# Kernel tuning notes

Measured on AMD Instinct MI355X. Metric: run time of the kernel, lower is better.

The kernel has to match this reference:

```python
import jax, jax.numpy as jnp
import numpy as np

B, S, H = 2, 2048, 1024
NQ, NKV, HD, RANK = 16, 4, 64, 8
THETA = 10000.0
LORA_SCALE = 16 / RANK  # alpha / rank = 2.0
ATTN_SCALE = 1.0 / np.sqrt(HD)


def setup_inputs() -> dict:
    key = jax.random.key(0)
    ks = jax.random.split(key, 14)
    n = lambda k, shape, s: jax.random.normal(k, shape, jnp.float32) * s
    return {
        "x": n(ks[0], (B, S, H), 1.0),
        # nn.Linear weights: [out_features, in_features], y = x @ W.T (scaled small for stability)
        "Wq": n(ks[1], (NQ * HD, H), 0.02),
        "Wk": n(ks[2], (NKV * HD, H), 0.02),
        "Wv": n(ks[3], (NKV * HD, H), 0.02),
        "Wo": n(ks[4], (H, NQ * HD), 0.02),
        "qA": n(ks[5], (RANK, H), 0.05), "qB": n(ks[6], (NQ * HD, RANK), 0.05),
        "kA": n(ks[7], (RANK, H), 0.05), "kB": n(ks[8], (NKV * HD, RANK), 0.05),
        "vA": n(ks[9], (RANK, H), 0.05), "vB": n(ks[10], (NKV * HD, RANK), 0.05),
        "oA": n(ks[11], (RANK, NQ * HD), 0.05), "oB": n(ks[12], (H, RANK), 0.05),
    }


def _lora_proj(x, W, A, Bm):
    # x @ W.T + ((x @ A.T) @ B.T) * lora_scaling
    return x @ W.T + ((x @ A.T) @ Bm.T) * LORA_SCALE


def _rope(x, cos_h, sin_h):
    # x: [b, h, s, d]; even/odd interleaved split, concatenated output (matches torch ref)
    x1, x2 = x[..., ::2], x[..., 1::2]
    return jnp.concatenate([x1 * cos_h - x2 * sin_h, x1 * sin_h + x2 * cos_h], axis=-1)


def _forward(x, Wq, Wk, Wv, Wo, qA, qB, kA, kB, vA, vB, oA, oB):
    b, s, _ = x.shape
    q = _lora_proj(x, Wq, qA, qB).reshape(b, s, NQ, HD).transpose(0, 2, 1, 3)
    k = _lora_proj(x, Wk, kA, kB).reshape(b, s, NKV, HD).transpose(0, 2, 1, 3)
    v = _lora_proj(x, Wv, vA, vB).reshape(b, s, NKV, HD).transpose(0, 2, 1, 3)

    inv_freq = 1.0 / (THETA ** (jnp.arange(0, HD, 2, dtype=jnp.float32) / HD))  # [HD/2]
    freqs = jnp.arange(s, dtype=jnp.float32)[:, None] * inv_freq[None, :]  # [s, HD/2]
    cos_h = jnp.cos(freqs)[None, None]  # [1,1,s,HD/2]
    sin_h = jnp.sin(freqs)[None, None]
    q = _rope(q, cos_h, sin_h)
    k = _rope(k, cos_h, sin_h)

    rep = NQ // NKV  # GQA: repeat_interleave along head axis
    k = jnp.repeat(k, rep, axis=1)
    v = jnp.repeat(v, rep, axis=1)

    attn = jax.nn.softmax(jnp.einsum('bhqd,bhkd->bhqk', q, k) * ATTN_SCALE, axis=-1)
    out = jnp.einsum('bhqk,bhkd->bhqd', attn, v)
    out = out.transpose(0, 2, 1, 3).reshape(b, s, NQ * HD)
    return _lora_proj(out, Wo, oA, oB)


def reference(x, Wq, Wk, Wv, Wo, qA, qB, kA, kB, vA, vB, oA, oB):
    return _forward(x, Wq, Wk, Wv, Wo, qA, qB, kA, kB, vA, vB, oA, oB)
```

## Files before the change

### kernel.cpp

```cpp
#include <hip/hip_runtime.h>

typedef _Float16 f16;
typedef __attribute__((ext_vector_type(8))) _Float16 f16x8;
typedef __attribute__((ext_vector_type(4))) float f32x4;

#define DI __device__ __forceinline__
#define MFMA16(a, b, c) __builtin_amdgcn_mfma_f32_16x16x32_f16(a, b, c, 0, 0, 0)

constexpr int BB = 2, SS = 2048, HH = 1024;
constexpr int NQ = 16, NKV = 4, HD = 64;
constexpr int NTOK = BB * SS;
constexpr int NQKV = NQ*HD + 2*NKV*HD;

DI f32x4 zero4() { f32x4 z = {0.f, 0.f, 0.f, 0.f}; return z; }

DI float fexp2(float x) {
#if __has_builtin(__builtin_amdgcn_exp2f)
  return __builtin_amdgcn_exp2f(x);
#else
  return exp2f(x);
#endif
}

DI unsigned pk2(float a, float b) {
#if __has_builtin(__builtin_amdgcn_cvt_pkrtz)
  typedef __fp16 fp16v2 __attribute__((ext_vector_type(2)));
  union { fp16v2 h; unsigned u; } c;
  c.h = __builtin_amdgcn_cvt_pkrtz(a, b);
  return c.u;
#else
  union { f16 h[2]; unsigned u; } c;
  c.h[0] = (f16)a; c.h[1] = (f16)b; return c.u;
#endif
}

DI void glds16(const void* g, void* l) {
  __builtin_amdgcn_global_load_lds((const __attribute__((address_space(1))) void*)g,
                                   (__attribute__((address_space(3))) void*)l, 16, 0, 0);
}

DI int shuf32(int i) {
  return (i & ~31) | (((i >> 2) & 3) << 3) | (i & 3) | (((i >> 4) & 1) << 2);
}

__global__ __launch_bounds__(256) void prep_kernel(
    const float* __restrict__ x,
    const float* __restrict__ Wq, const float* __restrict__ Wk,
    const float* __restrict__ Wv, const float* __restrict__ Wo,
    const float* __restrict__ qA, const float* __restrict__ qB,
    const float* __restrict__ kA, const float* __restrict__ kB,
    const float* __restrict__ vA, const float* __restrict__ vB,
    const float* __restrict__ oA, const float* __restrict__ oB,
    f16* __restrict__ xh, f16* __restrict__ Wqkv, f16* __restrict__ Woe,
    float* __restrict__ ctab, float* __restrict__ stab) {
  int idx = blockIdx.x * 256 + threadIdx.x;
  if (idx < NQKV * HH) {
    int n = idx >> 10, hcol = idx & 1023;
    const float *Am, *Bm; float wv; int nn;
    if (n < 1024)      { nn = n;        wv = Wq[idx];              Am = qA; Bm = qB; }
    else if (n < 1280) { nn = n - 1024; wv = Wk[nn*1024 + hcol];   Am = kA; Bm = kB; }
    else               { nn = n - 1280; wv = Wv[nn*1024 + hcol];   Am = vA; Bm = vB; }
    float s = 0.f;
#pragma unroll
    for (int r = 0; r < 8; ++r) s += Bm[nn*8 + r] * Am[r*1024 + hcol];
    Wqkv[shuf32(idx)] = (f16)(wv + 2.0f * s);
  } else if ((idx -= NQKV * HH) < 1024 * 1024) {
    int n = idx >> 10, hcol = idx & 1023;
    float s = 0.f;
#pragma unroll
    for (int r = 0; r < 8; ++r) s += oB[n*8 + r] * oA[r*1024 + hcol];
    Woe[shuf32(idx)] = (f16)(Wo[idx] + 2.0f * s);
  } else if ((idx -= 1024 * 1024) < NTOK * HH) {
    xh[shuf32(idx)] = (f16)x[idx];
  } else if ((idx -= NTOK * HH) < SS * 32) {
    int s = idx >> 5, d = idx & 31;
    float inv = expf(-(float)d * 0.28782313662425583f);
    float ang = (float)s * inv;
    ctab[idx] = cosf(ang);
    stab[idx] = sinf(ang);
  }
}

template<typename OUT_T>
__global__ __launch_bounds__(256, 2) void gemm_bt(const f16* __restrict__ A, const f16* __restrict__ Bw,
                                                  OUT_T* __restrict__ C, int M, int N, int K) {
  __shared__ char lds[65536];
  const int nt = N >> 7;
  const int nwg = (M >> 7) * nt;
  int bid = blockIdx.x;
  const int cpx = nwg >> 3;
  bid = (bid & 7) * cpx + (bid >> 3);
  const int m0 = (bid / nt) << 7;
  const int n0 = (bid % nt) << 7;
  const int tid = threadIdx.x;
  const int lane = tid & 63;
  const int w = tid >> 6, wr = w >> 1, wc = w & 1;
  const int l15 = lane & 15, g = (lane >> 4) & 3;
  const char* Ab = (const char*)A;
  const char* Bb = (const char*)Bw;
  const size_t Kb = (size_t)K * 2;
  const int srow = tid >> 3;
  const int scol = (tid & 7) << 4;

  auto stage = [&](int kt, int bs) {
    char* ab = lds + bs * 32768;
    char* bbuf = ab + 16384;
    const size_t kbyte = (size_t)kt << 7;
#pragma unroll
    for (int s = 0; s < 4; ++s) {
      int row = (s << 5) + srow;
      glds16(Ab + (size_t)(m0 + row) * Kb + kbyte + (scol ^ ((row & 7) << 4)),
             ab + (s << 12) + (w << 10));
    }
#pragma unroll
    for (int s = 0; s < 4; ++s) {
      int row = (s << 5) + srow;
      glds16(Bb + (size_t)(n0 + row) * Kb + kbyte + (scol ^ ((row & 7) << 4)),
             bbuf + (s << 12) + (w << 10));
    }
  };

  f32x4 acc[4][4];
#pragma unroll
  for (int i = 0; i < 4; ++i)
#pragma unroll
    for (int j = 0; j < 4; ++j) acc[i][j] = zero4();

  const int nkt = K >> 6;
  stage(0, 0);
  for (int t = 0; t < nkt; ++t) {
    __syncthreads();
    if (t + 1 < nkt) stage(t + 1, (t + 1) & 1);
    const char* ab = lds + (t & 1) * 32768;
    const char* bbuf = ab + 16384;
    f16x8 af[4][2], bf[4][2];
#pragma unroll
    for (int mi = 0; mi < 4; ++mi) {
      int ra = (wr << 6) + (mi << 4) + l15;
      int base = ra << 7, sw = (ra & 7) << 4;
#pragma unroll
      for (int kk = 0; kk < 2; ++kk)
        af[mi][kk] = *reinterpret_cast<const f16x8*>(ab + base + ((((kk << 6) + (g << 4))) ^ sw));
    }
#pragma unroll
    for (int nj = 0; nj < 4; ++nj) {
      int rb = (wc << 6) + (nj << 4) + l15;
      int base = rb << 7, sw = (rb & 7) << 4;
#pragma unroll
      for (int kk = 0; kk < 2; ++kk)
        bf[nj][kk] = *reinterpret_cast<const f16x8*>(bbuf + base + ((((kk << 6) + (g << 4))) ^ sw));
    }
#pragma unroll
    for (int mi = 0; mi < 4; ++mi)
#pragma unroll
      for (int nj = 0; nj < 4; ++nj) {
        acc[mi][nj] = MFMA16(af[mi][0], bf[nj][0], acc[mi][nj]);
        acc[mi][nj] = MFMA16(af[mi][1], bf[nj][1], acc[mi][nj]);
      }
  }
#pragma unroll
  for (int mi = 0; mi < 4; ++mi)
#pragma unroll
    for (int nj = 0; nj < 4; ++nj) {
      int mmb = m0 + (wr << 6) + (mi << 4) + (g << 2);
      int nn  = n0 + (wc << 6) + (nj << 4) + l15;
      f32x4 a = acc[mi][nj];
#pragma unroll
      for (int r = 0; r < 4; ++r) C[(size_t)(mmb + r) * N + nn] = (OUT_T)a[r];
    }
}

__global__ __launch_bounds__(256) void rope_kernel(const f16* __restrict__ qkv,
    const float* __restrict__ ctab, const float* __restrict__ stab,
    f16* __restrict__ Qr, f16* __restrict__ Kr) {
  int idx = blockIdx.x * 256 + threadIdx.x;
  int dp = idx & 31;
  int t = idx >> 5;
  int hh = t % 20;
  int tok = t / 20;
  int s = tok & (SS - 1), b = tok >> 11;
  float c  = ctab[(s << 5) + dp];
  float sn = stab[(s << 5) + dp];
  const f16* row = qkv + (size_t)tok * NQKV;
  int p1 = (((dp >> 2) & 3) << 3) | (dp & 3) | (((dp >> 4) & 1) << 2);
  if (hh < 16) {
    float x1 = (float)row[hh*64 + 2*dp], x2 = (float)row[hh*64 + 2*dp + 1];
    f16* out = Qr + ((size_t)(b*NQ + hh)*SS + s) * HD;
    constexpr float QS = 0.18033688011112042f;
    out[p1]      = (f16)(QS * (x1*c  - x2*sn));
    out[p1 + 32] = (f16)(QS * (x1*sn + x2*c));
  } else {
    int hk = hh - 16;
    float x1 = (float)row[1024 + hk*64 + 2*dp], x2 = (float)row[1024 + hk*64 + 2*dp + 1];
    f16* out = Kr + ((size_t)(b*NKV + hk)*SS + s) * HD;
    out[p1]      = (f16)(x1*c  - x2*sn);
    out[p1 + 32] = (f16)(x1*sn + x2*c);
  }
}

__global__ __launch_bounds__(256) void vtrans_kernel(const f16* __restrict__ qkv,
                                                     f16* __restrict__ Vt) {
  __shared__ f16 Ls[64 * 72];
  const int tid = threadIdx.x;
  const int blk = blockIdx.x;
  const int st = blk & 31, hkv = (blk >> 5) & 3, b = blk >> 7;
  const int s0 = st << 6;
  {
    int s = tid >> 2, d0 = (tid & 3) << 4;
    const f16* src = qkv + ((size_t)(b*SS + s0 + s)) * NQKV + 1280 + hkv*64 + d0;
    uint4 v0 = *reinterpret_cast<const uint4*>(src);
    uint4 v1 = *reinterpret_cast<const uint4*>(src + 8);
    *reinterpret_cast<uint4*>(Ls + s * 72 + d0) = v0;
    *reinterpret_cast<uint4*>(Ls + s * 72 + d0 + 8) = v1;
  }
  __syncthreads();
  int d = tid >> 2;
  f16* dst = Vt + ((size_t)(b*NKV + hkv)*64 + d) * SS + s0;
#pragma unroll
  for (int cc = 0; cc < 2; ++cc) {
    int cch = ((tid & 3) << 1) + cc;
    int m = cch >> 2, g = cch & 3;
    union { f16 h[8]; uint4 u; } o;
#pragma unroll
    for (int j = 0; j < 8; ++j) {
      int sl = (m << 5) + (g << 2) + (j & 3) + ((j >> 2) << 4);
      o.h[j] = Ls[sl * 72 + d];
    }
    *reinterpret_cast<uint4*>(dst + (cch << 3)) = o.u;
  }
}

__global__ __launch_bounds__(512, 4) void attn_kernel(
    const f16* __restrict__ Qr, const f16* __restrict__ Kr,
    const f16* __restrict__ Vt, f16* __restrict__ pacc0,
    f16* __restrict__ pacc1, float* __restrict__ pes) {
  __shared__ char lds[3 * 16384];
  const int tid = threadIdx.x, lane = tid & 63, w = tid >> 6;
  const int l15 = lane & 15, g = (lane >> 4) & 3;
  const int bh = blockIdx.x;
  const int b = bh >> 4, h = bh & 15, hkv = h >> 2;
  const int q0 = blockIdx.y << 8;
  const int split = blockIdx.z;
  const int kvbase = split << 10;
  const char* Kbase = (const char*)(Kr + (size_t)(b*NKV + hkv) * SS * HD);
  const char* Vbase = (const char*)(Vt + (size_t)(b*NKV + hkv) * HD * SS);

  f16x8 qf[2][2];
  {
    const f16* qr0 = Qr + ((size_t)(b*NQ + h)*SS + q0 + (w << 5) + l15) * HD + (g << 3);
    qf[0][0] = *reinterpret_cast<const f16x8*>(qr0);
    qf[0][1] = *reinterpret_cast<const f16x8*>(qr0 + 32);
    qf[1][0] = *reinterpret_cast<const f16x8*>(qr0 + 16*HD);
    qf[1][1] = *reinterpret_cast<const f16x8*>(qr0 + 16*HD + 32);
  }
  f16x8 ones;
#pragma unroll
  for (int i = 0; i < 8; ++i) ones[i] = (f16)1.0f;
  const f32x4 minit = {-4.f, -4.f, -4.f, -4.f};

  f32x4 acc[4][2];
#pragma unroll
  for (int i = 0; i < 4; ++i) { acc[i][0] = zero4(); acc[i][1] = zero4(); }
  f32x4 es0 = zero4(), es1 = zero4();

  const int srow = tid >> 3;
  const int scolb = (tid & 7) << 4;
  auto stage = [&](int kv0, int buf) {
    char* kb = lds + buf * 16384;
    char* vb = kb + 8192;
    glds16(Kbase + (size_t)(kv0 + srow) * 128 + (scolb ^ ((srow & 7) << 4)),
           kb + (w << 10));
    glds16(Vbase + (size_t)srow * 4096 + (kv0 << 1) + (scolb ^ ((srow & 7) << 4)),
           vb + (w << 10));
  };

  constexpr int NT = 16;
  stage(kvbase, 0);
  stage(kvbase + 64, 1);
  int cur = 0;

  for (int t = 0; t < NT; ++t) {
    if (t < NT - 1) asm volatile("s_waitcnt vmcnt(2)" ::: "memory");
    else            asm volatile("s_waitcnt vmcnt(0)" ::: "memory");
    __builtin_amdgcn_s_barrier();
    __builtin_amdgcn_sched_barrier(0);
    int nb = cur + 2; if (nb >= 3) nb -= 3;
    if (t + 2 < NT) stage(kvbase + ((t + 2) << 6), nb);

    const char* kb = lds + cur * 16384;
    const char* vb = kb + 8192;

    f32x4 sf0[4], sf1[4];
    __builtin_amdgcn_s_setprio(1);
#pragma unroll
    for (int mb = 0; mb < 4; ++mb) {
      int rowK = (mb << 4) + l15;
      int Bk = (rowK << 7) + ((g << 4) ^ ((rowK & 7) << 4));
      f16x8 kf0 = *reinterpret_cast<const f16x8*>(kb + Bk);
      f16x8 kf1 = *reinterpret_cast<const f16x8*>(kb + (Bk ^ 64));
      f32x4 z0 = minit, z1 = minit;
      z0 = MFMA16(kf0, qf[0][0], z0); z0 = MFMA16(kf1, qf[0][1], z0);
      z1 = MFMA16(kf0, qf[1][0], z1); z1 = MFMA16(kf1, qf[1][1], z1);
      sf0[mb] = z0; sf1[mb] = z1;
    }
    __builtin_amdgcn_s_setprio(0);

    union { unsigned u[8]; f16x8 v[2]; } p0, p1;
#pragma unroll
    for (int j = 0; j < 8; ++j) {
      int mb = j >> 1, r0 = (j & 1) << 1;
      p0.u[j] = pk2(fexp2(sf0[mb][r0]), fexp2(sf0[mb][r0 + 1]));
      p1.u[j] = pk2(fexp2(sf1[mb][r0]), fexp2(sf1[mb][r0 + 1]));
    }

    __builtin_amdgcn_s_setprio(1);
#pragma unroll
    for (int sh = 0; sh < 2; ++sh) {
#pragma unroll
      for (int db = 0; db < 4; ++db) {
        int rowV = (db << 4) + l15;
        int Bv = (rowV << 7) + ((g << 4) ^ ((rowV & 7) << 4));
        f16x8 vf = *reinterpret_cast<const f16x8*>(vb + (Bv ^ (sh << 6)));
        acc[db][0] = MFMA16(vf, p0.v[sh], acc[db][0]);
        acc[db][1] = MFMA16(vf, p1.v[sh], acc[db][1]);
      }
      es0 = MFMA16(ones, p0.v[sh], es0);
      es1 = MFMA16(ones, p1.v[sh], es1);
    }
    __builtin_amdgcn_s_setprio(0);

    cur += 1; if (cur == 3) cur = 0;
  }

  f16* pout = split ? pacc1 : pacc0;
  int sg0 = q0 + (w << 5) + l15;
  size_t ob0 = ((size_t)b * SS + sg0) * 1024 + h * 64;
  size_t ob1 = ob0 + (size_t)16 * 1024;
#pragma unroll
  for (int db = 0; db < 4; ++db) {
    union { f16 hv[4]; uint2 u; } o0, o1;
#pragma unroll
    for (int r = 0; r < 4; ++r) {
      o0.hv[r] = (f16)acc[db][0][r];
      o1.hv[r] = (f16)acc[db][1][r];
    }
    int pos = ((db >> 1) << 5) + (g << 3) + ((db & 1) << 2);
    *reinterpret_cast<uint2*>(pout + ob0 + pos) = o0.u;
    *reinterpret_cast<uint2*>(pout + ob1 + pos) = o1.u;
  }
  if (lane < 16) {
    int qv = q0 + (w << 5) + lane;
    float* pe = pes + ((size_t)(split*BB + b)*NQ + h)*SS;
    pe[qv] = es0[0];
    pe[qv + 16] = es1[0];
  }
}

__global__ __launch_bounds__(256) void combine_kernel(
    const f16* __restrict__ pacc0, const f16* __restrict__ pacc1,
    const float* __restrict__ pes, f16* __restrict__ AO) {
  int idx = blockIdx.x * 256 + threadIdx.x;
  int e = idx << 3;
  int tok = e >> 10;
  int col = e & 1023;
  int h = col >> 6;
  int b = tok >> 11, q = tok & (SS - 1);
  float e0 = pes[((size_t)(b)*NQ + h)*SS + q];
  float e1 = pes[((size_t)(BB + b)*NQ + h)*SS + q];
  float inv = 1.0f / (e0 + e1);
  union { uint4 u; f16 h8[8]; } a, c, o;
  a.u = *reinterpret_cast<const uint4*>(pacc0 + e);
  c.u = *reinterpret_cast<const uint4*>(pacc1 + e);
#pragma unroll
  for (int j = 0; j < 8; ++j)
    o.h8[j] = (f16)(((float)a.h8[j] + (float)c.h8[j]) * inv);
  *reinterpret_cast<uint4*>(AO + e) = o.u;
}

extern "C" void kernel_launch(void* const* d_in, const int* in_sizes, int n_in,
                              void* d_out, int out_size, void* d_ws, size_t ws_size,
                              hipStream_t stream) {
  const float* x  = (const float*)d_in[0];
  const float* Wq = (const float*)d_in[1];
  const float* Wk = (const float*)d_in[2];
  const float* Wv = (const float*)d_in[3];
  const float* Wo = (const float*)d_in[4];
  const float* qA = (const float*)d_in[5];
  const float* qB = (const float*)d_in[6];
  const float* kA = (const float*)d_in[7];
  const float* kB = (const float*)d_in[8];
  const float* vA = (const float*)d_in[9];
  const float* vB = (const float*)d_in[10];
  const float* oA = (const float*)d_in[11];
  const float* oB = (const float*)d_in[12];
  char* ws = (char*)d_ws;
  f16* xh    = (f16*)(ws);
  f16* Wqkv  = (f16*)(ws + 8388608);
  f16* Woe   = (f16*)(ws + 11534336);
  f16* qkv   = (f16*)(ws + 13631488);
  f16* Qr    = (f16*)(ws + 26214400);
  f16* Kr    = (f16*)(ws + 34603008);
  f16* Vt    = (f16*)(ws + 36700160);
  float* ctab = (float*)(ws + 38797312);
  float* stab = (float*)(ws + 39059456);
  f16* pacc0 = xh;
  f16* pacc1 = qkv;
  float* pes = (float*)(ws + 13631488 + 8388608);
  f16* AO = Qr;
  float* out = (float*)d_out;

  prep_kernel<<<26880, 256, 0, stream>>>(x, Wq, Wk, Wv, Wo, qA, qB, kA, kB, vA, vB, oA, oB,
                                         xh, Wqkv, Woe, ctab, stab);
  gemm_bt<f16><<<dim3(32 * 12), 256, 0, stream>>>(xh, Wqkv, qkv, 4096, 1536, 1024);
  rope_kernel<<<10240, 256, 0, stream>>>(qkv, ctab, stab, Qr, Kr);
  vtrans_kernel<<<256, 256, 0, stream>>>(qkv, Vt);
  attn_kernel<<<dim3(32, 8, 2), 512, 0, stream>>>(Qr, Kr, Vt, pacc0, pacc1, pes);
  combine_kernel<<<2048, 256, 0, stream>>>(pacc0, pacc1, pes, AO);
  gemm_bt<float><<<dim3(32 * 8), 256, 0, stream>>>(AO, Woe, out, 4096, 1024, 1024);
}
```

Before: 99.19 us.

## Process 64 query rows per wave in attention to double K/V fragment reuse

Each attention wave now handles four 16-row query tiles instead of two, so every K and V fragment read from LDS feeds twice as many MFMAs. The grid's query dimension is halved to match and the launch-bounds occupancy hint drops from 4 to 2 blocks per CU to make room for the larger accumulators. The exp2/pack step is also interleaved directly into the QK^T loop, and the setprio around the QK^T MFMAs is removed. In exchange, register pressure rises, fewer blocks are in flight (256 blocks total), and latency hiding is weaker.

```diff
diff --git a/kernel.cpp b/kernel.cpp
--- a/kernel.cpp
+++ b/kernel.cpp
@@ -230,7 +230,7 @@
   }
 }
 
-__global__ __launch_bounds__(512, 4) void attn_kernel(
+__global__ __launch_bounds__(512, 2) void attn_kernel(
     const f16* __restrict__ Qr, const f16* __restrict__ Kr,
     const f16* __restrict__ Vt, f16* __restrict__ pacc0,
     f16* __restrict__ pacc1, float* __restrict__ pes) {
@@ -239,29 +239,33 @@
   const int l15 = lane & 15, g = (lane >> 4) & 3;
   const int bh = blockIdx.x;
   const int b = bh >> 4, h = bh & 15, hkv = h >> 2;
-  const int q0 = blockIdx.y << 8;
+  const int q0 = blockIdx.y << 9;
+  const int wq = q0 + (w << 6);
   const int split = blockIdx.z;
   const int kvbase = split << 10;
   const char* Kbase = (const char*)(Kr + (size_t)(b*NKV + hkv) * SS * HD);
   const char* Vbase = (const char*)(Vt + (size_t)(b*NKV + hkv) * HD * SS);
 
-  f16x8 qf[2][2];
-  {
-    const f16* qr0 = Qr + ((size_t)(b*NQ + h)*SS + q0 + (w << 5) + l15) * HD + (g << 3);
-    qf[0][0] = *reinterpret_cast<const f16x8*>(qr0);
-    qf[0][1] = *reinterpret_cast<const f16x8*>(qr0 + 32);
-    qf[1][0] = *reinterpret_cast<const f16x8*>(qr0 + 16*HD);
-    qf[1][1] = *reinterpret_cast<const f16x8*>(qr0 + 16*HD + 32);
+  f16x8 qf[4][2];
+#pragma unroll
+  for (int qi = 0; qi < 4; ++qi) {
+    const f16* qr0 = Qr + ((size_t)(b*NQ + h)*SS + wq + (qi << 4) + l15) * HD + (g << 3);
+    qf[qi][0] = *reinterpret_cast<const f16x8*>(qr0);
+    qf[qi][1] = *reinterpret_cast<const f16x8*>(qr0 + 32);
   }
   f16x8 ones;
 #pragma unroll
   for (int i = 0; i < 8; ++i) ones[i] = (f16)1.0f;
   const f32x4 minit = {-4.f, -4.f, -4.f, -4.f};
 
-  f32x4 acc[4][2];
-#pragma unroll
-  for (int i = 0; i < 4; ++i) { acc[i][0] = zero4(); acc[i][1] = zero4(); }
-  f32x4 es0 = zero4(), es1 = zero4();
+  f32x4 acc[4][4];
+#pragma unroll
+  for (int i = 0; i < 4; ++i)
+#pragma unroll
+    for (int j = 0; j < 4; ++j) acc[i][j] = zero4();
+  f32x4 es[4];
+#pragma unroll
+  for (int i = 0; i < 4; ++i) es[i] = zero4();
 
   const int srow = tid >> 3;
   const int scolb = (tid & 7) << 4;
@@ -290,27 +294,21 @@
     const char* kb = lds + cur * 16384;
     const char* vb = kb + 8192;
 
-    f32x4 sf0[4], sf1[4];
-    __builtin_amdgcn_s_setprio(1);
+    union { unsigned u[8]; f16x8 v[2]; } p[4];
 #pragma unroll
     for (int mb = 0; mb < 4; ++mb) {
       int rowK = (mb << 4) + l15;
       int Bk = (rowK << 7) + ((g << 4) ^ ((rowK & 7) << 4));
       f16x8 kf0 = *reinterpret_cast<const f16x8*>(kb + Bk);
       f16x8 kf1 = *reinterpret_cast<const f16x8*>(kb + (Bk ^ 64));
-      f32x4 z0 = minit, z1 = minit;
-      z0 = MFMA16(kf0, qf[0][0], z0); z0 = MFMA16(kf1, qf[0][1], z0);
-      z1 = MFMA16(kf0, qf[1][0], z1); z1 = MFMA16(kf1, qf[1][1], z1);
-      sf0[mb] = z0; sf1[mb] = z1;
-    }
-    __builtin_amdgcn_s_setprio(0);
-
-    union { unsigned u[8]; f16x8 v[2]; } p0, p1;
-#pragma unroll
-    for (int j = 0; j < 8; ++j) {
-      int mb = j >> 1, r0 = (j & 1) << 1;
-      p0.u[j] = pk2(fexp2(sf0[mb][r0]), fexp2(sf0[mb][r0 + 1]));
-      p1.u[j] = pk2(fexp2(sf1[mb][r0]), fexp2(sf1[mb][r0 + 1]));
+#pragma unroll
+      for (int qi = 0; qi < 4; ++qi) {
+        f32x4 z = minit;
+        z = MFMA16(kf0, qf[qi][0], z);
+        z = MFMA16(kf1, qf[qi][1], z);
+        p[qi].u[(mb << 1)]     = pk2(fexp2(z[0]), fexp2(z[1]));
+        p[qi].u[(mb << 1) + 1] = pk2(fexp2(z[2]), fexp2(z[3]));
+      }
     }
 
     __builtin_amdgcn_s_setprio(1);
@@ -321,11 +319,13 @@
         int rowV = (db << 4) + l15;
         int Bv = (rowV << 7) + ((g << 4) ^ ((rowV & 7) << 4));
         f16x8 vf = *reinterpret_cast<const f16x8*>(vb + (Bv ^ (sh << 6)));
-        acc[db][0] = MFMA16(vf, p0.v[sh], acc[db][0]);
-        acc[db][1] = MFMA16(vf, p1.v[sh], acc[db][1]);
+#pragma unroll
+        for (int qi = 0; qi < 4; ++qi)
+          acc[db][qi] = MFMA16(vf, p[qi].v[sh], acc[db][qi]);
       }
-      es0 = MFMA16(ones, p0.v[sh], es0);
-      es1 = MFMA16(ones, p1.v[sh], es1);
+#pragma unroll
+      for (int qi = 0; qi < 4; ++qi)
+        es[qi] = MFMA16(ones, p[qi].v[sh], es[qi]);
     }
     __builtin_amdgcn_s_setprio(0);
 
@@ -333,26 +333,24 @@
   }
 
   f16* pout = split ? pacc1 : pacc0;
-  int sg0 = q0 + (w << 5) + l15;
-  size_t ob0 = ((size_t)b * SS + sg0) * 1024 + h * 64;
-  size_t ob1 = ob0 + (size_t)16 * 1024;
-#pragma unroll
-  for (int db = 0; db < 4; ++db) {
-    union { f16 hv[4]; uint2 u; } o0, o1;
-#pragma unroll
-    for (int r = 0; r < 4; ++r) {
-      o0.hv[r] = (f16)acc[db][0][r];
-      o1.hv[r] = (f16)acc[db][1][r];
-    }
-    int pos = ((db >> 1) << 5) + (g << 3) + ((db & 1) << 2);
-    *reinterpret_cast<uint2*>(pout + ob0 + pos) = o0.u;
-    *reinterpret_cast<uint2*>(pout + ob1 + pos) = o1.u;
+#pragma unroll
+  for (int qi = 0; qi < 4; ++qi) {
+    int sq = wq + (qi << 4) + l15;
+    size_t ob = ((size_t)b * SS + sq) * 1024 + h * 64;
+#pragma unroll
+    for (int db = 0; db < 4; ++db) {
+      union { f16 hv[4]; uint2 u; } o;
+#pragma unroll
+      for (int r = 0; r < 4; ++r) o.hv[r] = (f16)acc[db][qi][r];
+      int pos = ((db >> 1) << 5) + (g << 3) + ((db & 1) << 2);
+      *reinterpret_cast<uint2*>(pout + ob + pos) = o.u;
+    }
   }
   if (lane < 16) {
-    int qv = q0 + (w << 5) + lane;
     float* pe = pes + ((size_t)(split*BB + b)*NQ + h)*SS;
-    pe[qv] = es0[0];
-    pe[qv + 16] = es1[0];
+#pragma unroll
+    for (int qi = 0; qi < 4; ++qi)
+      pe[wq + (qi << 4) + lane] = es[qi][0];
   }
 }
 
@@ -414,7 +412,7 @@
   gemm_bt<f16><<<dim3(32 * 12), 256, 0, stream>>>(xh, Wqkv, qkv, 4096, 1536, 1024);
   rope_kernel<<<10240, 256, 0, stream>>>(qkv, ctab, stab, Qr, Kr);
   vtrans_kernel<<<256, 256, 0, stream>>>(qkv, Vt);
-  attn_kernel<<<dim3(32, 8, 2), 512, 0, stream>>>(Qr, Kr, Vt, pacc0, pacc1, pes);
+  attn_kernel<<<dim3(32, 4, 2), 512, 0, stream>>>(Qr, Kr, Vt, pacc0, pacc1, pes);
   combine_kernel<<<2048, 256, 0, stream>>>(pacc0, pacc1, pes, AO);
   gemm_bt<float><<<dim3(32 * 8), 256, 0, stream>>>(AO, Woe, out, 4096, 1024, 1024);
 }
```

Measured after the change: 100.6 us. About the same (+1.5%).
